# Performance work log

Hardware: AMD Instinct MI355X
Metric: run time of the kernel (lower is better)

Reference implementation:

```python
import jax, jax.numpy as jnp
import numpy as np
import math

B, H, L = 8, 256, 4096
C = 1            # channels
D_STATE = 64
DD = D_STATE // 2  # d = 32
DT_MIN, DT_MAX = 1e-3, 1e-1


def setup_inputs() -> dict:
    key = jax.random.key(0)
    ks = jax.random.split(key, 6)
    u = jax.random.normal(ks[0], (B, H, L), dtype=jnp.float32)
    # analytic init matching the torch module
    h_scale = jnp.exp(jnp.arange(H, dtype=jnp.float32) / H * math.log(DT_MAX / DT_MIN))  # (H,)
    angles = jnp.arange(DD, dtype=jnp.float32) * jnp.float32(np.pi)                      # (DD,)
    theta = jnp.einsum('c,h,d->chd', jnp.ones((C,), jnp.float32), h_scale, angles)       # (C,H,DD)
    a = -jnp.broadcast_to(h_scale[None, :, None], (C, H, DD)).astype(jnp.float32)        # (C,H,DD)
    D = jax.random.normal(ks[1], (C, H), dtype=jnp.float32)
    b_p = jax.random.normal(ks[2], (C, H, DD), dtype=jnp.float32)
    c_p = jax.random.normal(ks[3], (C, H, DD), dtype=jnp.float32)
    x0 = jax.random.normal(ks[4], (C, H, DD), dtype=jnp.float32)
    return {"u": u, "theta": theta, "a": a, "D": D, "b_p": b_p, "c_p": c_p, "x0": x0}


def fft_conv(u, f):
    # u: (B,H,L), f: (C,H,L) -> (B,C,H,L) causal conv via zero-padded FFT
    l = u.shape[-1]
    n = 2 * l
    u_f = jnp.fft.rfft(u, n=n)          # (B,H,n//2+1)
    f_f = jnp.fft.rfft(f, n=n)          # (C,H,n//2+1)
    y_f = jnp.einsum('bhl,chl->bchl', u_f, f_f)
    return jnp.fft.irfft(y_f, n=n)[..., :l]


def reference(u, theta, a, D, b_p, c_p, x0):
    l = u.shape[-1]
    T = 1.0 / (l - 1)
    zk = T * jnp.arange(l, dtype=jnp.float32)            # (L,)
    zk4 = zk[None, None, :, None]                         # (1,1,L,1)
    ls = -jnp.abs(a) + 1j * theta                         # (C,H,DD) complex
    term_0 = (jnp.exp(ls * T) - 1.0) / ls                 # (C,H,DD)
    # base_term: (C,H,L,DD)
    base_term = (2.0 * term_0[:, :, None, :] * jnp.exp(ls[:, :, None, :] * zk4)).real
    q = b_p * c_p                                         # (C,H,DD)
    f = jnp.einsum('chd,chld->chl', q, base_term)         # (C,H,L)
    y = fft_conv(u, f)                                    # (B,C,H,L)
    y = y + jnp.einsum('bhl,ch->bchl', u, D)
    # initial-condition term
    cos_term = 2.0 * T * jnp.exp(-jnp.abs(a)[:, :, None, :] * zk4) * jnp.cos(theta[:, :, None, :] * zk4)
    init = jnp.einsum('chd,chld->chl', 2.0 * (c_p * x0), cos_term)  # (C,H,L)
    y = y + init[None]                                    # broadcast over batch
    b = y.shape[0]
    return y.reshape(b, -1, l)                            # (B, C*H, L)
```

## Files before the change

kernel.cpp:

```cpp
#include <hip/hip_runtime.h>

#define BB 8
#define HH 256
#define LL 4096
#define STR 72

#define WS_H  0
#define WS_P  (2u*1024*1024)
#define WS_R  (4u*1024*1024)
#define WS_C1 (6u*1024*1024)
#define WS_C2 (6u*1024*1024 + 128u*1024)

typedef __attribute__((ext_vector_type(8))) short short8;
typedef __attribute__((ext_vector_type(4))) float f32x4;

static __device__ inline unsigned short f2bf(float x) {
    union { float f; unsigned u; } v; v.f = x;
    unsigned r = v.u + 0x7fffu + ((v.u >> 16) & 1u);
    return (unsigned short)(r >> 16);
}
static __device__ inline float bf2f(unsigned short us) {
    union { unsigned u; float f; } v; v.u = ((unsigned)us) << 16; return v.f;
}

#define CMUL(or_, oi_, ar_, ai_, br_, bi_) do { \
    float _tr = fmaf((ar_), (br_), -(ai_) * (bi_)); \
    float _ti = fmaf((ar_), (bi_), (ai_) * (br_)); \
    (or_) = _tr; (oi_) = _ti; } while (0)

__global__ __launch_bounds__(256) void s4_pre_kernel(
    const float* __restrict__ theta, const float* __restrict__ a,
    const float* __restrict__ b_p,   const float* __restrict__ c_p,
    const float* __restrict__ x0,
    unsigned short* __restrict__ Hm, unsigned short* __restrict__ Pm,
    unsigned short* __restrict__ Rm, float4* __restrict__ C1,
    float* __restrict__ C2)
{
    const int tid = threadIdx.x;
    const int h   = blockIdx.x;
    const int d   = tid & 31;
    const int kb  = tid >> 5;
    const float T = 1.0f / (LL - 1);
    __shared__ float h_s[64];

    const float lr = a[h * 32 + d];
    const float li = theta[h * 32 + d];
    float sn, cS;
    sincosf(li * T, &sn, &cS);
    const float er = expf(lr * T);
    const float Rr = er * cS, Ri = er * sn;
    const float den = lr * lr + li * li;
    const float t0r = ((Rr - 1.f) * lr + Ri * li) / den;
    const float t0i = (Ri * lr - (Rr - 1.f) * li) / den;
    const float qq  = b_p[h * 32 + d] * c_p[h * 32 + d];
    const float wre = 2.f * qq * t0r, wim = 2.f * qq * t0i;
    const float vv  = 4.f * T * c_p[h * 32 + d] * x0[h * 32 + d];

    float r2r, r2i, r4r, r4i, r8r, r8i, r16r, r16i, r32r, r32i;
    CMUL(r2r, r2i, Rr, Ri, Rr, Ri);
    CMUL(r4r, r4i, r2r, r2i, r2r, r2i);
    CMUL(r8r, r8i, r4r, r4i, r4r, r4i);
    CMUL(r16r, r16i, r8r, r8i, r8r, r8i);
    CMUL(r32r, r32i, r16r, r16i, r16r, r16i);

    unsigned short* HmB = Hm + h * 4096;
    unsigned short* PmB = Pm + h * 4096;
    unsigned short* RmB = Rm + h * 4096;

    {
        float pr = 1.f, pi = 0.f;
        if (kb & 1) CMUL(pr, pi, pr, pi, r8r, r8i);
        if (kb & 2) CMUL(pr, pi, pr, pi, r16r, r16i);
        if (kb & 4) CMUL(pr, pi, pr, pi, r32r, r32i);
        #pragma unroll
        for (int k8 = 0; k8 < 8; ++k8) {
            const int k = (kb << 3) + k8;
            RmB[k * 64 + d]           = f2bf(pr);
            RmB[k * 64 + 32 + d]      = f2bf(-pi);
            PmB[d * 64 + (63 - k)]        = f2bf(pr);
            PmB[(32 + d) * 64 + (63 - k)] = f2bf(pi);
            float hk = fmaf(wre, pr, -wim * pi);
            hk += __shfl_xor(hk, 1);
            hk += __shfl_xor(hk, 2);
            hk += __shfl_xor(hk, 4);
            hk += __shfl_xor(hk, 8);
            hk += __shfl_xor(hk, 16);
            if (d == 0) h_s[k] = hk;
            CMUL(pr, pi, pr, pi, Rr, Ri);
        }
    }
    if (tid < 32) {
        float Ar, Ai, wrr, wri;
        CMUL(Ar, Ai, r32r, r32i, r32r, r32i);
        CMUL(wrr, wri, wre, wim, Rr, Ri);
        C1[h * 32 + d] = make_float4(Ar, Ai, wrr, wri);
        C2[h * 32 + d] = vv;
    }
    __syncthreads();

    {
        const int t  = tid >> 2;
        const int tb = (tid & 3) << 4;
        #pragma unroll
        for (int g = 0; g < 4; ++g) {
            const int tau0 = tb + (g << 2);
            unsigned short e[4];
            #pragma unroll
            for (int i = 0; i < 4; ++i) {
                const int dt = t - (tau0 + i);
                e[i] = (dt >= 0) ? f2bf(h_s[dt]) : (unsigned short)0;
            }
            uint2 pk;
            pk.x = (unsigned)e[0] | ((unsigned)e[1] << 16);
            pk.y = (unsigned)e[2] | ((unsigned)e[3] << 16);
            *(uint2*)&HmB[t * 64 + tau0] = pk;
        }
    }
}

__global__ __launch_bounds__(256, 4) void s4_main_kernel(
    const float* __restrict__ u, const float* __restrict__ Dp,
    const unsigned short* __restrict__ Hm, const unsigned short* __restrict__ Pm,
    const unsigned short* __restrict__ Rm, const float4* __restrict__ C1,
    const float* __restrict__ C2, float* __restrict__ out)
{
    const int tid = threadIdx.x;
    const int blk = blockIdx.x;
    const int hh  = blk >> 2;
    const int bp  = blk & 3;

    __shared__ __align__(16) short UsA[64 * STR];
    __shared__ __align__(16) short UsB[64 * STR];
    __shared__ __align__(16) short EQ[64 * STR];
    __shared__ __align__(16) float Seg[32 * 18];

    const int d    = tid & 31;
    const int g    = tid >> 5;
    const int ln   = tid & 63;
    const int m0   = (tid >> 6) << 4;
    const int rowi = ln & 15;
    const int quad = ln >> 4;

    const unsigned short* HmB = Hm + hh * 4096;
    const unsigned short* PmB = Pm + hh * 4096;
    const unsigned short* RmB = Rm + hh * 4096;
    short8 aH[2], aP[2], aR[2];
    #pragma unroll
    for (int kh = 0; kh < 2; ++kh) {
        const int off = (m0 + rowi) * 64 + (kh << 5) + (quad << 3);
        aH[kh] = *(const short8*)&HmB[off];
        aP[kh] = *(const short8*)&PmB[off];
        aR[kh] = *(const short8*)&RmB[off];
    }

    const float* up0 = u + ((((size_t)(bp * 2) * HH) + hh) << 12);
    const float* up1 = u + ((((size_t)(bp * 2 + 1) * HH) + hh) << 12);
    #pragma unroll
    for (int jj = 0; jj < 4; ++jj) {
        const int v  = tid + (jj << 8);
        const float4 val = ((const float4*)up0)[v];
        const int c  = v >> 4;
        const int t0 = (v & 15) << 2;
        uint2 pk;
        pk.x = (unsigned)f2bf(val.x) | ((unsigned)f2bf(val.y) << 16);
        pk.y = (unsigned)f2bf(val.z) | ((unsigned)f2bf(val.w) << 16);
        *(uint2*)&UsA[c * STR + t0] = pk;
    }
    float4 v1[4];
    #pragma unroll
    for (int jj = 0; jj < 4; ++jj)
        v1[jj] = ((const float4*)up1)[tid + (jj << 8)];

    const float4 c1 = C1[hh * 32 + d];
    const float vv  = C2[hh * 32 + d];
    const float Dh  = Dp[hh];
    const float Ar = c1.x, Ai = c1.y;
    float S8r, S8i, S16r, S16i, S32r, S32i;
    {
        float b1r, b1i, b2r, b2i;
        CMUL(b1r, b1i, Ar, Ai, Ar, Ai);
        CMUL(b2r, b2i, b1r, b1i, b1r, b1i);
        CMUL(S8r, S8i, b2r, b2i, b2r, b2i);
        CMUL(S16r, S16i, S8r, S8i, S8r, S8i);
        CMUL(S32r, S32i, S16r, S16i, S16r, S16i);
    }
    __syncthreads();

    #pragma unroll
    for (int it = 0; it < 2; ++it) {
        short* Us = it ? UsB : UsA;

        f32x4 accY[4], accE[4];
        #pragma unroll
        for (int nt = 0; nt < 4; ++nt) {
            accY[nt] = (f32x4){0.f, 0.f, 0.f, 0.f};
            accE[nt] = (f32x4){0.f, 0.f, 0.f, 0.f};
        }
        #pragma unroll
        for (int kh = 0; kh < 2; ++kh) {
            const int k0 = kh << 5;
            #pragma unroll
            for (int nt = 0; nt < 4; ++nt) {
                const short8 bU = *(const short8*)&Us[((nt << 4) + rowi) * STR + k0 + (quad << 3)];
                accY[nt] = __builtin_amdgcn_mfma_f32_16x16x32_bf16(aH[kh], bU, accY[nt], 0, 0, 0);
                accE[nt] = __builtin_amdgcn_mfma_f32_16x16x32_bf16(aP[kh], bU, accE[nt], 0, 0, 0);
            }
        }

        #pragma unroll
        for (int nt = 0; nt < 4; ++nt) {
            uint2 pk;
            pk.x = (unsigned)f2bf(accE[nt][0]) | ((unsigned)f2bf(accE[nt][1]) << 16);
            pk.y = (unsigned)f2bf(accE[nt][2]) | ((unsigned)f2bf(accE[nt][3]) << 16);
            *(uint2*)&EQ[((nt << 4) + rowi) * STR + m0 + (quad << 2)] = pk;
        }

        if (it == 0) {
            #pragma unroll
            for (int jj = 0; jj < 4; ++jj) {
                const int v  = tid + (jj << 8);
                const int c  = v >> 4;
                const int t0 = (v & 15) << 2;
                uint2 pk;
                pk.x = (unsigned)f2bf(v1[jj].x) | ((unsigned)f2bf(v1[jj].y) << 16);
                pk.y = (unsigned)f2bf(v1[jj].z) | ((unsigned)f2bf(v1[jj].w) << 16);
                *(uint2*)&UsB[c * STR + t0] = pk;
            }
        }
        __syncthreads();

        const int cb = g << 3;
        float Er[8], Ei[8];
        {
            float Sr = 0.f, Si = 0.f;
            #pragma unroll
            for (int i = 0; i < 8; ++i) {
                const int c = cb + i;
                Er[i] = bf2f((unsigned short)EQ[c * STR + d]);
                Ei[i] = bf2f((unsigned short)EQ[c * STR + 32 + d]);
                const float nr = fmaf(Ar, Sr, fmaf(-Ai, Si, Er[i]));
                const float ni = fmaf(Ar, Si, fmaf(Ai, Sr, Ei[i]));
                Sr = nr; Si = ni;
            }
            Seg[d * 18 + (g << 1)]     = Sr;
            Seg[d * 18 + (g << 1) + 1] = Si;
        }
        __syncthreads();

        {
            float offr = 0.f, offi = 0.f;
            #pragma unroll
            for (int gp = 0; gp < 7; ++gp) {
                const float2 sg = *(const float2*)&Seg[d * 18 + (gp << 1)];
                const float nr = fmaf(S8r, offr, fmaf(-S8i, offi, sg.x));
                const float ni = fmaf(S8r, offi, fmaf(S8i, offr, sg.y));
                const bool take = gp < g;
                offr = take ? nr : offr;
                offi = take ? ni : offi;
            }
            float Gr = vv, Gi = 0.f;
            if (g & 1) { float nr, ni; CMUL(nr, ni, Gr, Gi, S8r, S8i);   Gr = nr; Gi = ni; }
            if (g & 2) { float nr, ni; CMUL(nr, ni, Gr, Gi, S16r, S16i); Gr = nr; Gi = ni; }
            if (g & 4) { float nr, ni; CMUL(nr, ni, Gr, Gi, S32r, S32i); Gr = nr; Gi = ni; }
            const float wrr = c1.z, wri = c1.w;
            float Sr = offr, Si = offi;
            #pragma unroll
            for (int i = 0; i < 8; ++i) {
                const int c = cb + i;
                const float Qr = fmaf(wrr, Sr, fmaf(-wri, Si, Gr));
                const float Qi = fmaf(wrr, Si, fmaf(wri, Sr, Gi));
                EQ[c * STR + d]      = (short)f2bf(Qr);
                EQ[c * STR + 32 + d] = (short)f2bf(Qi);
                const float nr = fmaf(Ar, Sr, fmaf(-Ai, Si, Er[i]));
                const float ni = fmaf(Ar, Si, fmaf(Ai, Sr, Ei[i]));
                Sr = nr; Si = ni;
                float nGr, nGi;
                CMUL(nGr, nGi, Ar, Ai, Gr, Gi);
                Gr = nGr; Gi = nGi;
            }
        }
        __syncthreads();

        #pragma unroll
        for (int kh = 0; kh < 2; ++kh) {
            const int k0 = kh << 5;
            #pragma unroll
            for (int nt = 0; nt < 4; ++nt) {
                const short8 bQ = *(const short8*)&EQ[((nt << 4) + rowi) * STR + k0 + (quad << 3)];
                accY[nt] = __builtin_amdgcn_mfma_f32_16x16x32_bf16(aR[kh], bQ, accY[nt], 0, 0, 0);
            }
        }

        float* op = out + ((((size_t)(bp * 2 + it) * HH) + hh) << 12);
        #pragma unroll
        for (int nt = 0; nt < 4; ++nt) {
            const int c    = (nt << 4) + rowi;
            const int toff = m0 + (quad << 2);
            const uint2 uu = *(const uint2*)&Us[c * STR + toff];
            float4 res;
            res.x = fmaf(Dh, bf2f((unsigned short)(uu.x & 0xffffu)), accY[nt][0]);
            res.y = fmaf(Dh, bf2f((unsigned short)(uu.x >> 16)),     accY[nt][1]);
            res.z = fmaf(Dh, bf2f((unsigned short)(uu.y & 0xffffu)), accY[nt][2]);
            res.w = fmaf(Dh, bf2f((unsigned short)(uu.y >> 16)),     accY[nt][3]);
            *(float4*)&op[c * 64 + toff] = res;
        }
        __syncthreads();
    }
}

extern "C" void kernel_launch(void* const* d_in, const int* in_sizes, int n_in,
                              void* d_out, int out_size, void* d_ws, size_t ws_size,
                              hipStream_t stream) {
    const float* u     = (const float*)d_in[0];
    const float* theta = (const float*)d_in[1];
    const float* a     = (const float*)d_in[2];
    const float* Dp    = (const float*)d_in[3];
    const float* b_p   = (const float*)d_in[4];
    const float* c_p   = (const float*)d_in[5];
    const float* x0    = (const float*)d_in[6];
    float* out = (float*)d_out;
    char* ws = (char*)d_ws;
    unsigned short* Hm = (unsigned short*)(ws + WS_H);
    unsigned short* Pm = (unsigned short*)(ws + WS_P);
    unsigned short* Rm = (unsigned short*)(ws + WS_R);
    float4*         C1 = (float4*)(ws + WS_C1);
    float*          C2 = (float*)(ws + WS_C2);

    hipLaunchKernelGGL(s4_pre_kernel, dim3(HH), dim3(256), 0, stream,
                       theta, a, b_p, c_p, x0, Hm, Pm, Rm, C1, C2);
    hipLaunchKernelGGL(s4_main_kernel, dim3(HH * 4), dim3(256), 0, stream,
                       u, Dp, Hm, Pm, Rm, C1, C2, out);
}
```

Before: 104.6 us.

## Fold D skip into Toeplitz diagonal and interleave both batch items per block

The D·u skip term is folded into the first coefficient of the intra-chunk Toeplitz matrix, which removes the epilogue FMA and the need to keep u in LDS for it. The main kernel now processes its two batch items together instead of in a sequential loop: both u loads are issued up front, the MFMAs are interleaved, and the scan and state propagation run on both at once. EQ is dropped and the UsA/UsB buffers are reused for the E and Q matrices, cutting barriers in half and reducing LDS footprint. In exchange, register pressure rises with doubled accumulators and Er/Ei arrays, and D now passes through bf16 rounding of the Toeplitz entry.

```diff
diff --git a/kernel.cpp b/kernel.cpp
--- a/kernel.cpp
+++ b/kernel.cpp
@@ -1,6 +1,5 @@
 #include <hip/hip_runtime.h>
 
-#define BB 8
 #define HH 256
 #define LL 4096
 #define STR 72
@@ -31,7 +30,7 @@
 __global__ __launch_bounds__(256) void s4_pre_kernel(
     const float* __restrict__ theta, const float* __restrict__ a,
     const float* __restrict__ b_p,   const float* __restrict__ c_p,
-    const float* __restrict__ x0,
+    const float* __restrict__ x0,    const float* __restrict__ Dp,
     unsigned short* __restrict__ Hm, unsigned short* __restrict__ Pm,
     unsigned short* __restrict__ Rm, float4* __restrict__ C1,
     float* __restrict__ C2)
@@ -45,6 +44,7 @@
 
     const float lr = a[h * 32 + d];
     const float li = theta[h * 32 + d];
+    const float Dh = Dp[h];
     float sn, cS;
     sincosf(li * T, &sn, &cS);
     const float er = expf(lr * T);
@@ -85,7 +85,7 @@
             hk += __shfl_xor(hk, 4);
             hk += __shfl_xor(hk, 8);
             hk += __shfl_xor(hk, 16);
-            if (d == 0) h_s[k] = hk;
+            if (d == 0) h_s[k] = hk + ((k == 0) ? Dh : 0.f);
             CMUL(pr, pi, pr, pi, Rr, Ri);
         }
     }
@@ -119,7 +119,7 @@
 }
 
 __global__ __launch_bounds__(256, 4) void s4_main_kernel(
-    const float* __restrict__ u, const float* __restrict__ Dp,
+    const float* __restrict__ u,
     const unsigned short* __restrict__ Hm, const unsigned short* __restrict__ Pm,
     const unsigned short* __restrict__ Rm, const float4* __restrict__ C1,
     const float* __restrict__ C2, float* __restrict__ out)
@@ -131,8 +131,7 @@
 
     __shared__ __align__(16) short UsA[64 * STR];
     __shared__ __align__(16) short UsB[64 * STR];
-    __shared__ __align__(16) short EQ[64 * STR];
-    __shared__ __align__(16) float Seg[32 * 18];
+    __shared__ __align__(16) float Seg[2][32 * 18];
 
     const int d    = tid & 31;
     const int g    = tid >> 5;
@@ -155,25 +154,27 @@
 
     const float* up0 = u + ((((size_t)(bp * 2) * HH) + hh) << 12);
     const float* up1 = u + ((((size_t)(bp * 2 + 1) * HH) + hh) << 12);
+    float4 v0[4], v1[4];
+    #pragma unroll
+    for (int jj = 0; jj < 4; ++jj) v0[jj] = ((const float4*)up0)[tid + (jj << 8)];
+    #pragma unroll
+    for (int jj = 0; jj < 4; ++jj) v1[jj] = ((const float4*)up1)[tid + (jj << 8)];
     #pragma unroll
     for (int jj = 0; jj < 4; ++jj) {
         const int v  = tid + (jj << 8);
-        const float4 val = ((const float4*)up0)[v];
         const int c  = v >> 4;
         const int t0 = (v & 15) << 2;
         uint2 pk;
-        pk.x = (unsigned)f2bf(val.x) | ((unsigned)f2bf(val.y) << 16);
-        pk.y = (unsigned)f2bf(val.z) | ((unsigned)f2bf(val.w) << 16);
+        pk.x = (unsigned)f2bf(v0[jj].x) | ((unsigned)f2bf(v0[jj].y) << 16);
+        pk.y = (unsigned)f2bf(v0[jj].z) | ((unsigned)f2bf(v0[jj].w) << 16);
         *(uint2*)&UsA[c * STR + t0] = pk;
-    }
-    float4 v1[4];
-    #pragma unroll
-    for (int jj = 0; jj < 4; ++jj)
-        v1[jj] = ((const float4*)up1)[tid + (jj << 8)];
+        pk.x = (unsigned)f2bf(v1[jj].x) | ((unsigned)f2bf(v1[jj].y) << 16);
+        pk.y = (unsigned)f2bf(v1[jj].z) | ((unsigned)f2bf(v1[jj].w) << 16);
+        *(uint2*)&UsB[c * STR + t0] = pk;
+    }
 
     const float4 c1 = C1[hh * 32 + d];
     const float vv  = C2[hh * 32 + d];
-    const float Dh  = Dp[hh];
     const float Ar = c1.x, Ai = c1.y;
     float S8r, S8i, S16r, S16i, S32r, S32i;
     {
@@ -186,125 +187,136 @@
     }
     __syncthreads();
 
-    #pragma unroll
-    for (int it = 0; it < 2; ++it) {
-        short* Us = it ? UsB : UsA;
-
-        f32x4 accY[4], accE[4];
+    f32x4 accY0[4], accE0[4], accY1[4], accE1[4];
+    #pragma unroll
+    for (int nt = 0; nt < 4; ++nt) {
+        accY0[nt] = (f32x4){0.f, 0.f, 0.f, 0.f};
+        accE0[nt] = (f32x4){0.f, 0.f, 0.f, 0.f};
+        accY1[nt] = (f32x4){0.f, 0.f, 0.f, 0.f};
+        accE1[nt] = (f32x4){0.f, 0.f, 0.f, 0.f};
+    }
+    #pragma unroll
+    for (int kh = 0; kh < 2; ++kh) {
+        const int k0 = kh << 5;
         #pragma unroll
         for (int nt = 0; nt < 4; ++nt) {
-            accY[nt] = (f32x4){0.f, 0.f, 0.f, 0.f};
-            accE[nt] = (f32x4){0.f, 0.f, 0.f, 0.f};
-        }
-        #pragma unroll
-        for (int kh = 0; kh < 2; ++kh) {
-            const int k0 = kh << 5;
-            #pragma unroll
-            for (int nt = 0; nt < 4; ++nt) {
-                const short8 bU = *(const short8*)&Us[((nt << 4) + rowi) * STR + k0 + (quad << 3)];
-                accY[nt] = __builtin_amdgcn_mfma_f32_16x16x32_bf16(aH[kh], bU, accY[nt], 0, 0, 0);
-                accE[nt] = __builtin_amdgcn_mfma_f32_16x16x32_bf16(aP[kh], bU, accE[nt], 0, 0, 0);
-            }
-        }
-
+            const int boff = ((nt << 4) + rowi) * STR + k0 + (quad << 3);
+            const short8 bU0 = *(const short8*)&UsA[boff];
+            const short8 bU1 = *(const short8*)&UsB[boff];
+            accY0[nt] = __builtin_amdgcn_mfma_f32_16x16x32_bf16(aH[kh], bU0, accY0[nt], 0, 0, 0);
+            accE0[nt] = __builtin_amdgcn_mfma_f32_16x16x32_bf16(aP[kh], bU0, accE0[nt], 0, 0, 0);
+            accY1[nt] = __builtin_amdgcn_mfma_f32_16x16x32_bf16(aH[kh], bU1, accY1[nt], 0, 0, 0);
+            accE1[nt] = __builtin_amdgcn_mfma_f32_16x16x32_bf16(aP[kh], bU1, accE1[nt], 0, 0, 0);
+        }
+    }
+    __syncthreads();
+
+    #pragma unroll
+    for (int nt = 0; nt < 4; ++nt) {
+        const int eoff = ((nt << 4) + rowi) * STR + m0 + (quad << 2);
+        uint2 pk;
+        pk.x = (unsigned)f2bf(accE0[nt][0]) | ((unsigned)f2bf(accE0[nt][1]) << 16);
+        pk.y = (unsigned)f2bf(accE0[nt][2]) | ((unsigned)f2bf(accE0[nt][3]) << 16);
+        *(uint2*)&UsA[eoff] = pk;
+        pk.x = (unsigned)f2bf(accE1[nt][0]) | ((unsigned)f2bf(accE1[nt][1]) << 16);
+        pk.y = (unsigned)f2bf(accE1[nt][2]) | ((unsigned)f2bf(accE1[nt][3]) << 16);
+        *(uint2*)&UsB[eoff] = pk;
+    }
+    __syncthreads();
+
+    const int cb = g << 3;
+    float Er[2][8], Ei[2][8];
+    {
+        float Sr0 = 0.f, Si0 = 0.f, Sr1 = 0.f, Si1 = 0.f;
+        #pragma unroll
+        for (int i = 0; i < 8; ++i) {
+            const int c = cb + i;
+            Er[0][i] = bf2f((unsigned short)UsA[c * STR + d]);
+            Ei[0][i] = bf2f((unsigned short)UsA[c * STR + 32 + d]);
+            Er[1][i] = bf2f((unsigned short)UsB[c * STR + d]);
+            Ei[1][i] = bf2f((unsigned short)UsB[c * STR + 32 + d]);
+            float nr = fmaf(Ar, Sr0, fmaf(-Ai, Si0, Er[0][i]));
+            float ni = fmaf(Ar, Si0, fmaf(Ai, Sr0, Ei[0][i]));
+            Sr0 = nr; Si0 = ni;
+            nr = fmaf(Ar, Sr1, fmaf(-Ai, Si1, Er[1][i]));
+            ni = fmaf(Ar, Si1, fmaf(Ai, Sr1, Ei[1][i]));
+            Sr1 = nr; Si1 = ni;
+        }
+        Seg[0][d * 18 + (g << 1)]     = Sr0;
+        Seg[0][d * 18 + (g << 1) + 1] = Si0;
+        Seg[1][d * 18 + (g << 1)]     = Sr1;
+        Seg[1][d * 18 + (g << 1) + 1] = Si1;
+    }
+    __syncthreads();
+
+    {
+        float offr0 = 0.f, offi0 = 0.f, offr1 = 0.f, offi1 = 0.f;
+        #pragma unroll
+        for (int gp = 0; gp < 7; ++gp) {
+            const float2 s0 = *(const float2*)&Seg[0][d * 18 + (gp << 1)];
+            const float2 s1 = *(const float2*)&Seg[1][d * 18 + (gp << 1)];
+            const bool take = gp < g;
+            float nr = fmaf(S8r, offr0, fmaf(-S8i, offi0, s0.x));
+            float ni = fmaf(S8r, offi0, fmaf(S8i, offr0, s0.y));
+            offr0 = take ? nr : offr0; offi0 = take ? ni : offi0;
+            nr = fmaf(S8r, offr1, fmaf(-S8i, offi1, s1.x));
+            ni = fmaf(S8r, offi1, fmaf(S8i, offr1, s1.y));
+            offr1 = take ? nr : offr1; offi1 = take ? ni : offi1;
+        }
+        float Gr = vv, Gi = 0.f;
+        if (g & 1) { float nr, ni; CMUL(nr, ni, Gr, Gi, S8r, S8i);   Gr = nr; Gi = ni; }
+        if (g & 2) { float nr, ni; CMUL(nr, ni, Gr, Gi, S16r, S16i); Gr = nr; Gi = ni; }
+        if (g & 4) { float nr, ni; CMUL(nr, ni, Gr, Gi, S32r, S32i); Gr = nr; Gi = ni; }
+        const float wrr = c1.z, wri = c1.w;
+        float Gr1 = Gr, Gi1 = Gi;
+        #pragma unroll
+        for (int i = 0; i < 8; ++i) {
+            const int c = cb + i;
+            float Qr = fmaf(wrr, offr0, fmaf(-wri, offi0, Gr));
+            float Qi = fmaf(wrr, offi0, fmaf(wri, offr0, Gi));
+            UsA[c * STR + d]      = (short)f2bf(Qr);
+            UsA[c * STR + 32 + d] = (short)f2bf(Qi);
+            Qr = fmaf(wrr, offr1, fmaf(-wri, offi1, Gr1));
+            Qi = fmaf(wrr, offi1, fmaf(wri, offr1, Gi1));
+            UsB[c * STR + d]      = (short)f2bf(Qr);
+            UsB[c * STR + 32 + d] = (short)f2bf(Qi);
+            float nr = fmaf(Ar, offr0, fmaf(-Ai, offi0, Er[0][i]));
+            float ni = fmaf(Ar, offi0, fmaf(Ai, offr0, Ei[0][i]));
+            offr0 = nr; offi0 = ni;
+            nr = fmaf(Ar, offr1, fmaf(-Ai, offi1, Er[1][i]));
+            ni = fmaf(Ar, offi1, fmaf(Ai, offr1, Ei[1][i]));
+            offr1 = nr; offi1 = ni;
+            float nGr, nGi;
+            CMUL(nGr, nGi, Ar, Ai, Gr, Gi);
+            Gr = nGr; Gi = nGi;
+            CMUL(nGr, nGi, Ar, Ai, Gr1, Gi1);
+            Gr1 = nGr; Gi1 = nGi;
+        }
+    }
+    __syncthreads();
+
+    #pragma unroll
+    for (int kh = 0; kh < 2; ++kh) {
+        const int k0 = kh << 5;
         #pragma unroll
         for (int nt = 0; nt < 4; ++nt) {
-            uint2 pk;
-            pk.x = (unsigned)f2bf(accE[nt][0]) | ((unsigned)f2bf(accE[nt][1]) << 16);
-            pk.y = (unsigned)f2bf(accE[nt][2]) | ((unsigned)f2bf(accE[nt][3]) << 16);
-            *(uint2*)&EQ[((nt << 4) + rowi) * STR + m0 + (quad << 2)] = pk;
-        }
-
-        if (it == 0) {
-            #pragma unroll
-            for (int jj = 0; jj < 4; ++jj) {
-                const int v  = tid + (jj << 8);
-                const int c  = v >> 4;
-                const int t0 = (v & 15) << 2;
-                uint2 pk;
-                pk.x = (unsigned)f2bf(v1[jj].x) | ((unsigned)f2bf(v1[jj].y) << 16);
-                pk.y = (unsigned)f2bf(v1[jj].z) | ((unsigned)f2bf(v1[jj].w) << 16);
-                *(uint2*)&UsB[c * STR + t0] = pk;
-            }
-        }
-        __syncthreads();
-
-        const int cb = g << 3;
-        float Er[8], Ei[8];
-        {
-            float Sr = 0.f, Si = 0.f;
-            #pragma unroll
-            for (int i = 0; i < 8; ++i) {
-                const int c = cb + i;
-                Er[i] = bf2f((unsigned short)EQ[c * STR + d]);
-                Ei[i] = bf2f((unsigned short)EQ[c * STR + 32 + d]);
-                const float nr = fmaf(Ar, Sr, fmaf(-Ai, Si, Er[i]));
-                const float ni = fmaf(Ar, Si, fmaf(Ai, Sr, Ei[i]));
-                Sr = nr; Si = ni;
-            }
-            Seg[d * 18 + (g << 1)]     = Sr;
-            Seg[d * 18 + (g << 1) + 1] = Si;
-        }
-        __syncthreads();
-
-        {
-            float offr = 0.f, offi = 0.f;
-            #pragma unroll
-            for (int gp = 0; gp < 7; ++gp) {
-                const float2 sg = *(const float2*)&Seg[d * 18 + (gp << 1)];
-                const float nr = fmaf(S8r, offr, fmaf(-S8i, offi, sg.x));
-                const float ni = fmaf(S8r, offi, fmaf(S8i, offr, sg.y));
-                const bool take = gp < g;
-                offr = take ? nr : offr;
-                offi = take ? ni : offi;
-            }
-            float Gr = vv, Gi = 0.f;
-            if (g & 1) { float nr, ni; CMUL(nr, ni, Gr, Gi, S8r, S8i);   Gr = nr; Gi = ni; }
-            if (g & 2) { float nr, ni; CMUL(nr, ni, Gr, Gi, S16r, S16i); Gr = nr; Gi = ni; }
-            if (g & 4) { float nr, ni; CMUL(nr, ni, Gr, Gi, S32r, S32i); Gr = nr; Gi = ni; }
-            const float wrr = c1.z, wri = c1.w;
-            float Sr = offr, Si = offi;
-            #pragma unroll
-            for (int i = 0; i < 8; ++i) {
-                const int c = cb + i;
-                const float Qr = fmaf(wrr, Sr, fmaf(-wri, Si, Gr));
-                const float Qi = fmaf(wrr, Si, fmaf(wri, Sr, Gi));
-                EQ[c * STR + d]      = (short)f2bf(Qr);
-                EQ[c * STR + 32 + d] = (short)f2bf(Qi);
-                const float nr = fmaf(Ar, Sr, fmaf(-Ai, Si, Er[i]));
-                const float ni = fmaf(Ar, Si, fmaf(Ai, Sr, Ei[i]));
-                Sr = nr; Si = ni;
-                float nGr, nGi;
-                CMUL(nGr, nGi, Ar, Ai, Gr, Gi);
-                Gr = nGr; Gi = nGi;
-            }
-        }
-        __syncthreads();
-
-        #pragma unroll
-        for (int kh = 0; kh < 2; ++kh) {
-            const int k0 = kh << 5;
-            #pragma unroll
-            for (int nt = 0; nt < 4; ++nt) {
-                const short8 bQ = *(const short8*)&EQ[((nt << 4) + rowi) * STR + k0 + (quad << 3)];
-                accY[nt] = __builtin_amdgcn_mfma_f32_16x16x32_bf16(aR[kh], bQ, accY[nt], 0, 0, 0);
-            }
-        }
-
-        float* op = out + ((((size_t)(bp * 2 + it) * HH) + hh) << 12);
-        #pragma unroll
-        for (int nt = 0; nt < 4; ++nt) {
-            const int c    = (nt << 4) + rowi;
-            const int toff = m0 + (quad << 2);
-            const uint2 uu = *(const uint2*)&Us[c * STR + toff];
-            float4 res;
-            res.x = fmaf(Dh, bf2f((unsigned short)(uu.x & 0xffffu)), accY[nt][0]);
-            res.y = fmaf(Dh, bf2f((unsigned short)(uu.x >> 16)),     accY[nt][1]);
-            res.z = fmaf(Dh, bf2f((unsigned short)(uu.y & 0xffffu)), accY[nt][2]);
-            res.w = fmaf(Dh, bf2f((unsigned short)(uu.y >> 16)),     accY[nt][3]);
-            *(float4*)&op[c * 64 + toff] = res;
-        }
-        __syncthreads();
+            const int boff = ((nt << 4) + rowi) * STR + k0 + (quad << 3);
+            const short8 bQ0 = *(const short8*)&UsA[boff];
+            const short8 bQ1 = *(const short8*)&UsB[boff];
+            accY0[nt] = __builtin_amdgcn_mfma_f32_16x16x32_bf16(aR[kh], bQ0, accY0[nt], 0, 0, 0);
+            accY1[nt] = __builtin_amdgcn_mfma_f32_16x16x32_bf16(aR[kh], bQ1, accY1[nt], 0, 0, 0);
+        }
+    }
+    float* op0 = out + ((((size_t)(bp * 2) * HH) + hh) << 12);
+    float* op1 = out + ((((size_t)(bp * 2 + 1) * HH) + hh) << 12);
+    #pragma unroll
+    for (int nt = 0; nt < 4; ++nt) {
+        const int c    = (nt << 4) + rowi;
+        const int toff = m0 + (quad << 2);
+        *(float4*)&op0[c * 64 + toff] =
+            make_float4(accY0[nt][0], accY0[nt][1], accY0[nt][2], accY0[nt][3]);
+        *(float4*)&op1[c * 64 + toff] =
+            make_float4(accY1[nt][0], accY1[nt][1], accY1[nt][2], accY1[nt][3]);
     }
 }
 
@@ -327,7 +339,7 @@
     float*          C2 = (float*)(ws + WS_C2);
 
     hipLaunchKernelGGL(s4_pre_kernel, dim3(HH), dim3(256), 0, stream,
-                       theta, a, b_p, c_p, x0, Hm, Pm, Rm, C1, C2);
+                       theta, a, b_p, c_p, x0, Dp, Hm, Pm, Rm, C1, C2);
     hipLaunchKernelGGL(s4_main_kernel, dim3(HH * 4), dim3(256), 0, stream,
-                       u, Dp, Hm, Pm, Rm, C1, C2, out);
-}
+                       u, Hm, Pm, Rm, C1, C2, out);
+}
```

Measured after the change: 107.2 us. 1.02x slower.
